# Kernel tuning notes

Hardware: AMD Instinct MI355X
Metric: run time of the kernel (lower is better)

The kernel has to match this reference:

```python
import math
import jax, jax.numpy as jnp
import numpy as np

B, N, D = 32, 1025, 768
K, CD, TD = 64, 128, 256  # num_clusters, cluster_dim, token_dim
REG = 0.1
NUM_ITERS = 5


def setup_inputs() -> dict:
    key = jax.random.key(0)
    ks = jax.random.split(key, 8)
    x = jax.random.normal(ks[0], (B, N, D), dtype=jnp.float32)
    # Linear params (torch nn.Linear: y = x @ W.T + b; we store W already transposed as [in, out])
    Wf = jax.random.normal(ks[1], (D, CD), dtype=jnp.float32) / math.sqrt(D)
    bf = jnp.zeros((CD,), dtype=jnp.float32)
    Ws = jax.random.normal(ks[2], (D, K), dtype=jnp.float32) / math.sqrt(D)
    bs = jnp.zeros((K,), dtype=jnp.float32)
    Wt = jax.random.normal(ks[3], (D, TD), dtype=jnp.float32) / math.sqrt(D)
    bt = jnp.zeros((TD,), dtype=jnp.float32)
    anchors = jax.random.normal(ks[4], (K, CD), dtype=jnp.float32) * 0.1
    dust_bin = jnp.float32(1.0)
    sharpness = jnp.float32(5.0)
    return {"x": x, "Wf": Wf, "bf": bf, "Ws": Ws, "bs": bs, "Wt": Wt, "bt": bt,
            "anchors": anchors, "dust_bin": dust_bin, "sharpness": sharpness}


def _log_otp_solver(log_a, log_b, M, num_iters, reg):
    M = M / reg
    u = jnp.zeros_like(log_a)  # [B, K+1]
    v = jnp.zeros_like(log_b)  # [B, N-1]
    for _ in range(num_iters):
        u = log_a - jax.nn.logsumexp(M + v[:, None, :], axis=2)
        v = log_b - jax.nn.logsumexp(M + u[:, :, None], axis=1)
    return M + u[:, :, None] + v[:, None, :]


def reference(x, Wf, bf, Ws, bs, Wt, bt, anchors, dust_bin, sharpness):
    b, n, d = x.shape
    t_global = x[:, 0]            # [B, D]
    fi = x[:, 1:]                 # [B, N-1, D]
    f = fi @ Wf + bf              # [B, N-1, CD]
    s = jnp.swapaxes(fi @ Ws + bs, 1, 2)  # [B, K, N-1]
    t = t_global @ Wt + bt        # [B, TD]
    s = s * sharpness
    dust = jnp.broadcast_to(dust_bin, (b, 1, n - 1))
    s_aug = jnp.concatenate([s, dust], axis=1)  # [B, K+1, N-1]
    log_a = jnp.full((b, K + 1), -math.log(K + 1), dtype=x.dtype)
    log_b = jnp.full((b, n - 1), -math.log(n - 1), dtype=x.dtype)
    log_P = _log_otp_solver(log_a, log_b, s_aug, NUM_ITERS, REG)
    p = jnp.exp(log_P)[:, :-1, :]  # [B, K, N-1]
    # v_agg = sum_n p[b,k,n] * (2*f[b,n,:] - anchors[k,:])  (algebraic rewrite of the broadcast sum)
    v_agg = 2.0 * jnp.einsum('bkn,bnc->bkc', p, f) - p.sum(axis=2)[:, :, None] * anchors[None]
    v_local = v_agg.reshape(b, -1)            # [B, K*CD]
    f_out = jnp.concatenate([t, v_local], axis=-1)
    norm = jnp.maximum(jnp.linalg.norm(f_out, axis=-1, keepdims=True), 1e-12)
    return f_out / norm
```

## Files before the change

### kernel.cpp

```cpp
#include <hip/hip_runtime.h>
#include <math.h>


#define BATCH 32
#define NTOK  1025
#define DIM   768
#define KDIM  64
#define CDIM  128
#define TDIM  256
#define NM1   1024
#define ROWLEN 8448
#define NITER 5
#define INV_REG 10.0f
#define NSPLIT 32
#define LOG_A (-4.17438727f)
#define LOG_B (-6.93147181f)

typedef __attribute__((ext_vector_type(8))) short short8;
typedef __attribute__((ext_vector_type(4))) float floatx4;

typedef __attribute__((address_space(3))) unsigned int lds_uint;
typedef const __attribute__((address_space(1))) unsigned int glb_uint;

__device__ __forceinline__ void gload_lds16(const void* g, void* l) {
    __builtin_amdgcn_global_load_lds((glb_uint*)g, (lds_uint*)l, 16, 0, 0);
}

__device__ __forceinline__ unsigned short bf16_rne(float f) {
    unsigned u = __builtin_bit_cast(unsigned, f);
    unsigned r = u + 0x7FFFu + ((u >> 16) & 1u);
    return (unsigned short)(r >> 16);
}

__device__ __forceinline__ short8 cvt8(float4 a, float4 b) {
    short8 r;
    r[0] = (short)bf16_rne(a.x); r[1] = (short)bf16_rne(a.y);
    r[2] = (short)bf16_rne(a.z); r[3] = (short)bf16_rne(a.w);
    r[4] = (short)bf16_rne(b.x); r[5] = (short)bf16_rne(b.y);
    r[6] = (short)bf16_rne(b.z); r[7] = (short)bf16_rne(b.w);
    return r;
}

__global__ __launch_bounds__(256) void pack_w(
    const float* __restrict__ Wf, const float* __restrict__ Ws,
    const float* __restrict__ bf, const float* __restrict__ bs,
    short* __restrict__ W_pack, float* __restrict__ bias_all)
{
    int idx = blockIdx.x * 256 + threadIdx.x;
    if (idx < 24 * 12 * 512) {
        int g    = idx / 6144;
        int rem  = idx - g * 6144;
        int nf   = rem >> 9;
        int rem2 = rem & 511;
        int lane = rem2 >> 3;
        int j    = rem2 & 7;
        int k = g * 32 + (lane >> 4) * 8 + j;
        int c = nf * 16 + (lane & 15);
        float v = (c < CDIM) ? Wf[(size_t)k * CDIM + c] : Ws[(size_t)k * KDIM + (c - CDIM)];
        W_pack[idx] = (short)bf16_rne(v);
    }
    if (idx < 192) bias_all[idx] = (idx < CDIM) ? bf[idx] : bs[idx - CDIM];
}

__global__ __launch_bounds__(256, 2) void gemm_fs(
    const float* __restrict__ x, const short* __restrict__ W_pack,
    const float* __restrict__ bias_all, const float* __restrict__ sharp_p,
    float* __restrict__ fmat, float* __restrict__ Mmat)
{
    __shared__ __align__(16) short Bs[12288];
    __shared__ __align__(16) short As[4096];
    const int tid  = threadIdx.x;
    const int wave = tid >> 6, lane = tid & 63;
    const int quad = lane >> 4, lrow = lane & 15;
    const int R = blockIdx.x * 64 + wave * 16;

    const int arow = blockIdx.x * 64 + (tid >> 2);
    const float* asrc = x + ((size_t)(arow >> 10) * NTOK + 1 + (arow & 1023)) * DIM + (tid & 3) * 16;
    const int r    = (tid >> 2) & 15;
    const int seg  = tid & 3;
    const int kk_w = seg >> 1;
    const int q0   = (seg & 1) * 2;
    short* adst0 = &As[(((tid >> 6) * 2 + kk_w) * 64 + q0 * 16 + r) * 8];
    short* adst1 = &As[(((tid >> 6) * 2 + kk_w) * 64 + (q0 + 1) * 16 + r) * 8];

    floatx4 acc[12];
#pragma unroll
    for (int nf = 0; nf < 12; ++nf) acc[nf] = (floatx4){0.f, 0.f, 0.f, 0.f};

    float4 g0 = *(const float4*)(asrc);
    float4 g1 = *(const float4*)(asrc + 4);
    float4 g2 = *(const float4*)(asrc + 8);
    float4 g3 = *(const float4*)(asrc + 12);

    for (int ko = 0; ko < 12; ++ko) {
        __syncthreads();
        const short* bsrc = W_pack + ko * 12288 + tid * 8;
#pragma unroll
        for (int i = 0; i < 6; ++i)
            gload_lds16(bsrc + i * 2048, &Bs[i * 2048 + tid * 8]);
        *(short8*)adst0 = cvt8(g0, g1);
        *(short8*)adst1 = cvt8(g2, g3);
        if (ko < 11) {
            const float* ap = asrc + (ko + 1) * 64;
            g0 = *(const float4*)(ap);
            g1 = *(const float4*)(ap + 4);
            g2 = *(const float4*)(ap + 8);
            g3 = *(const float4*)(ap + 12);
        }
        __syncthreads();
#pragma unroll
        for (int kk = 0; kk < 2; ++kk) {
            short8 af = *(const short8*)&As[((wave * 2 + kk) * 64 + lane) * 8];
#pragma unroll
            for (int nf = 0; nf < 12; ++nf) {
                short8 bf8 = *(const short8*)&Bs[((kk * 12 + nf) * 64 + lane) * 8];
                acc[nf] = __builtin_amdgcn_mfma_f32_16x16x32_bf16(af, bf8, acc[nf], 0, 0, 0);
            }
        }
    }

    const float sc = sharp_p[0] * INV_REG;
    const int bb = R >> 10;
    const int n0 = (R & 1023) + quad * 4;
#pragma unroll
    for (int nf = 0; nf < 12; ++nf) {
        const int c = nf * 16 + lrow;
        const float bias = bias_all[c];
        if (nf < 8) {
            float* fp = fmat + ((size_t)R + quad * 4) * CDIM + c;
#pragma unroll
            for (int j = 0; j < 4; ++j)
                fp[(size_t)j * CDIM] = acc[nf][j] + bias;
        } else {
            const int k = c - CDIM;
            float4 w = make_float4((acc[nf][0] + bias) * sc, (acc[nf][1] + bias) * sc,
                                   (acc[nf][2] + bias) * sc, (acc[nf][3] + bias) * sc);
            *(float4*)(Mmat + ((size_t)bb * KDIM + k) * NM1 + n0) = w;
        }
    }
}

__global__ __launch_bounds__(256) void gemm_t_split(
    const float* __restrict__ x, const float* __restrict__ Wt,
    float* __restrict__ tpart)
{
    __shared__ float xr[256];
    const int b = blockIdx.x, dy = blockIdx.y, c = threadIdx.x;
    xr[c] = x[(size_t)b * NTOK * DIM + (size_t)dy * 256 + c];
    __syncthreads();
    float acc = 0.f;
    const float* wp = Wt + (size_t)dy * 256 * TDIM + c;
#pragma unroll 8
    for (int d = 0; d < 256; ++d) acc = fmaf(xr[d], wp[(size_t)d * TDIM], acc);
    tpart[((size_t)dy * BATCH + b) * TDIM + c] = acc;
}

template<bool FIRST>
__global__ __launch_bounds__(256) void sink_u(
    const float* __restrict__ Mmat, const float* __restrict__ v_in,
    const float* __restrict__ dust_p, float* __restrict__ u_out)
{
    const int wv   = (blockIdx.x << 2) + (threadIdx.x >> 6);
    const int lane = threadIdx.x & 63;
    const int b = wv / 65, k = wv - b * 65;
    const float dustM = dust_p[0] * INV_REG;

    const float4* vp = (const float4*)(v_in + (size_t)b * NM1);
    float xs[16];
    if (k < 64) {
        const float4* Mp = (const float4*)(Mmat + ((size_t)b * KDIM + k) * NM1);
#pragma unroll
        for (int i = 0; i < 4; ++i) {
            float4 mv = Mp[i * 64 + lane];
            float4 vv = FIRST ? make_float4(0.f, 0.f, 0.f, 0.f) : vp[i * 64 + lane];
            xs[i * 4 + 0] = mv.x + vv.x;
            xs[i * 4 + 1] = mv.y + vv.y;
            xs[i * 4 + 2] = mv.z + vv.z;
            xs[i * 4 + 3] = mv.w + vv.w;
        }
    } else {
#pragma unroll
        for (int i = 0; i < 4; ++i) {
            float4 vv = FIRST ? make_float4(0.f, 0.f, 0.f, 0.f) : vp[i * 64 + lane];
            xs[i * 4 + 0] = dustM + vv.x;
            xs[i * 4 + 1] = dustM + vv.y;
            xs[i * 4 + 2] = dustM + vv.z;
            xs[i * 4 + 3] = dustM + vv.w;
        }
    }
    float m = xs[0];
#pragma unroll
    for (int i = 1; i < 16; ++i) m = fmaxf(m, xs[i]);
#pragma unroll
    for (int off = 1; off < 64; off <<= 1) m = fmaxf(m, __shfl_xor(m, off));
    float S = 0.f;
#pragma unroll
    for (int i = 0; i < 16; ++i) S += __expf(xs[i] - m);
#pragma unroll
    for (int off = 1; off < 64; off <<= 1) S += __shfl_xor(S, off);
    if (lane == 0) u_out[wv] = LOG_A - (m + __logf(S));
}

__global__ __launch_bounds__(128) void sink_v(
    const float* __restrict__ Mmat, const float* __restrict__ u_in,
    const float* __restrict__ dust_p, float* __restrict__ v_out)
{
    __shared__ float us[65];
    const int b = blockIdx.x, tid = threadIdx.x;
    const int n = blockIdx.y * 128 + tid;
    if (tid < 65) us[tid] = u_in[b * 65 + tid];
    __syncthreads();
    const float* Mb = Mmat + (size_t)b * KDIM * NM1 + n;
    float xs[64];
#pragma unroll
    for (int k = 0; k < 64; ++k) xs[k] = Mb[(size_t)k * NM1] + us[k];
    const float xd = dust_p[0] * INV_REG + us[64];
    float m = xd;
#pragma unroll
    for (int k = 0; k < 64; ++k) m = fmaxf(m, xs[k]);
    float S = __expf(xd - m);
#pragma unroll
    for (int k = 0; k < 64; ++k) S += __expf(xs[k] - m);
    v_out[(size_t)b * NM1 + n] = LOG_B - (m + __logf(S));
}

__global__ __launch_bounds__(256) void aggregate(
    const float* __restrict__ Mmat, const float* __restrict__ fmat,
    const float* __restrict__ u_in, const float* __restrict__ v_in,
    float* __restrict__ vpart, float* __restrict__ rspart)
{
    __shared__ float fs[32 * 128];
    __shared__ float ps[32 * 68];
    __shared__ float us[KDIM];
    __shared__ float vsh[32];
    const int b = blockIdx.x, ns = blockIdx.y;
    const int tid = threadIdx.x;
    const int tx = tid & 7;
    const int ty = tid >> 3;
    const int n0 = ns * 32;

    if (tid < 64) us[tid] = u_in[b * 65 + tid];
    else if (tid < 96) vsh[tid - 64] = v_in[(size_t)b * NM1 + n0 + (tid - 64)];
    __syncthreads();

    const float* fb = fmat + ((size_t)b * NM1 + n0) * CDIM;
#pragma unroll
    for (int q = 0; q < 4; ++q) {
        int idx = q * 256 + tid;
        int nn = idx >> 5, c4 = (idx & 31) * 4;
        *(float4*)&fs[nn * 128 + c4] = *(const float4*)(fb + (size_t)nn * CDIM + c4);
    }
    {
        const int p_nn = tid & 31, p_kb = tid >> 5;
        const float* Mb = Mmat + (size_t)b * KDIM * NM1 + n0 + p_nn;
        const float vv = vsh[p_nn];
#pragma unroll
        for (int q = 0; q < 8; ++q) {
            int k = q * 8 + p_kb;
            ps[p_nn * 68 + k] = __expf(Mb[(size_t)k * NM1] + us[k] + vv);
        }
    }
    __syncthreads();

    float rsacc = 0.f;
    if (tid < 64) {
#pragma unroll
        for (int nn = 0; nn < 32; ++nn) rsacc += ps[nn * 68 + tid];
    }
    float acc[8][4];
#pragma unroll
    for (int i = 0; i < 8; ++i)
#pragma unroll
        for (int j = 0; j < 4; ++j) acc[i][j] = 0.f;
#pragma unroll
    for (int nn = 0; nn < 32; ++nn) {
        float4 p0 = *(const float4*)&ps[nn * 68 + tx * 8];
        float4 p1 = *(const float4*)&ps[nn * 68 + tx * 8 + 4];
        float4 f0 = *(const float4*)&fs[nn * 128 + ty * 4];
        float pv[8] = {p0.x, p0.y, p0.z, p0.w, p1.x, p1.y, p1.z, p1.w};
        float fv[4] = {f0.x, f0.y, f0.z, f0.w};
#pragma unroll
        for (int i = 0; i < 8; ++i)
#pragma unroll
            for (int j = 0; j < 4; ++j)
                acc[i][j] = fmaf(pv[i], fv[j], acc[i][j]);
    }

    float* vp = vpart + (size_t)(ns * BATCH + b) * (KDIM * CDIM);
#pragma unroll
    for (int i = 0; i < 8; ++i) {
        int k = tx * 8 + i;
        *(float4*)(vp + (size_t)k * CDIM + ty * 4) =
            make_float4(acc[i][0], acc[i][1], acc[i][2], acc[i][3]);
    }
    if (tid < 64) rspart[(ns * BATCH + b) * KDIM + tid] = rsacc;
}

__global__ __launch_bounds__(256) void reduce_vagg(
    const float* __restrict__ vpart, const float* __restrict__ rspart,
    const float* __restrict__ anchors, float* __restrict__ vagg,
    float* __restrict__ sq)
{
    __shared__ float rst[8];
    __shared__ float red[4];
    const int b = blockIdx.x, segi = blockIdx.y, tid = threadIdx.x;
    const int lane = tid & 63, wave = tid >> 6;
    if (tid < 8) {
        float s = 0.f;
#pragma unroll
        for (int ns = 0; ns < NSPLIT; ++ns)
            s += rspart[(ns * BATCH + b) * KDIM + segi * 8 + tid];
        rst[tid] = s;
    }
    __syncthreads();
    const int i4 = segi * 256 + tid;
    float4 s = make_float4(0.f, 0.f, 0.f, 0.f);
#pragma unroll
    for (int ns = 0; ns < NSPLIT; ++ns) {
        const float4 v = *(const float4*)&vpart[(size_t)(ns * BATCH + b) * (KDIM * CDIM) + (size_t)i4 * 4];
        s.x += v.x; s.y += v.y; s.z += v.z; s.w += v.w;
    }
    float rs = rst[tid >> 5];
    const float4 an = *(const float4*)&anchors[(size_t)i4 * 4];
    float4 v;
    v.x = 2.f * s.x - rs * an.x;
    v.y = 2.f * s.y - rs * an.y;
    v.z = 2.f * s.z - rs * an.z;
    v.w = 2.f * s.w - rs * an.w;
    *(float4*)&vagg[(size_t)b * (KDIM * CDIM) + (size_t)i4 * 4] = v;
    float ss = v.x * v.x + v.y * v.y + v.z * v.z + v.w * v.w;
#pragma unroll
    for (int off = 32; off > 0; off >>= 1) ss += __shfl_down(ss, off);
    if (lane == 0) red[wave] = ss;
    __syncthreads();
    if (tid == 0) sq[b * 8 + segi] = red[0] + red[1] + red[2] + red[3];
}

__global__ __launch_bounds__(256) void finalize2(
    const float* __restrict__ tpart, const float* __restrict__ bt,
    const float* __restrict__ sq, const float* __restrict__ vagg,
    float* __restrict__ out)
{
    __shared__ float red[4];
    __shared__ float sc_sh;
    const int b = blockIdx.x, tid = threadIdx.x;
    const int lane = tid & 63, wave = tid >> 6;

    float t = bt[tid];
#pragma unroll
    for (int s = 0; s < 3; ++s) t += tpart[((size_t)s * BATCH + b) * TDIM + tid];
    float ss = t * t;
#pragma unroll
    for (int off = 32; off > 0; off >>= 1) ss += __shfl_down(ss, off);
    if (lane == 0) red[wave] = ss;
    __syncthreads();
    if (tid == 0) {
        float tot = red[0] + red[1] + red[2] + red[3];
#pragma unroll
        for (int i = 0; i < 8; ++i) tot += sq[b * 8 + i];
        sc_sh = 1.f / fmaxf(sqrtf(tot), 1e-12f);
    }
    __syncthreads();
    const float scale = sc_sh;
    float* orow = out + (size_t)b * ROWLEN;
    orow[tid] = t * scale;
    const float* va = vagg + (size_t)b * (KDIM * CDIM);
#pragma unroll
    for (int q = 0; q < 8; ++q) {
        int i4 = q * 256 + tid;
        float4 v = *(const float4*)&va[(size_t)i4 * 4];
        v.x *= scale; v.y *= scale; v.z *= scale; v.w *= scale;
        *(float4*)&orow[TDIM + (size_t)i4 * 4] = v;
    }
}

extern "C" void kernel_launch(void* const* d_in, const int* in_sizes, int n_in,
                              void* d_out, int out_size, void* d_ws, size_t ws_size,
                              hipStream_t stream)
{
    const float* x       = (const float*)d_in[0];
    const float* Wf      = (const float*)d_in[1];
    const float* bf      = (const float*)d_in[2];
    const float* Ws      = (const float*)d_in[3];
    const float* bs      = (const float*)d_in[4];
    const float* Wt      = (const float*)d_in[5];
    const float* bt      = (const float*)d_in[6];
    const float* anchors = (const float*)d_in[7];
    const float* dust    = (const float*)d_in[8];
    const float* sharp   = (const float*)d_in[9];
    float* out = (float*)d_out;

    char* base = (char*)d_ws;
    short* W_pack   = (short*)base;
    float* bias_all = (float*)(base + 294912);
    float* Mmat     = bias_all + 192;
    float* fmat     = Mmat + (size_t)BATCH * KDIM * NM1;
    float* u_buf    = fmat + (size_t)BATCH * NM1 * CDIM;
    float* v_buf    = u_buf + BATCH * 65;
    float* vpart    = v_buf + BATCH * NM1;
    float* rspart   = vpart + (size_t)NSPLIT * BATCH * KDIM * CDIM;
    float* tpart    = rspart + NSPLIT * BATCH * KDIM;
    float* sq       = tpart + 3 * BATCH * TDIM;
    float* vagg     = Mmat;

    hipLaunchKernelGGL(pack_w, dim3(576), dim3(256), 0, stream,
                       Wf, Ws, bf, bs, W_pack, bias_all);
    hipLaunchKernelGGL(gemm_fs, dim3(512), dim3(256), 0, stream,
                       x, W_pack, bias_all, sharp, fmat, Mmat);
    hipLaunchKernelGGL(gemm_t_split, dim3(BATCH, 3), dim3(256), 0, stream,
                       x, Wt, tpart);

    hipLaunchKernelGGL(HIP_KERNEL_NAME(sink_u<true>), dim3(520), dim3(256), 0, stream,
                       Mmat, v_buf, dust, u_buf);
    hipLaunchKernelGGL(sink_v, dim3(BATCH, 8), dim3(128), 0, stream,
                       Mmat, u_buf, dust, v_buf);
    for (int it = 1; it < NITER; ++it) {
        hipLaunchKernelGGL(HIP_KERNEL_NAME(sink_u<false>), dim3(520), dim3(256), 0, stream,
                           Mmat, v_buf, dust, u_buf);
        hipLaunchKernelGGL(sink_v, dim3(BATCH, 8), dim3(128), 0, stream,
                           Mmat, u_buf, dust, v_buf);
    }

    hipLaunchKernelGGL(aggregate, dim3(BATCH, NSPLIT), dim3(256), 0, stream,
                       Mmat, fmat, u_buf, v_buf, vpart, rspart);
    hipLaunchKernelGGL(reduce_vagg, dim3(BATCH, 8), dim3(256), 0, stream,
                       vpart, rspart, anchors, vagg, sq);
    hipLaunchKernelGGL(finalize2, dim3(BATCH), dim3(256), 0, stream,
                       tpart, bt, sq, vagg, out);
}
```

Before: 248.1 us.

## Use bf16 MFMA in aggregate with transposed bf16 features and fused finalize

The f projection is stored as transposed bf16 (fT), so the aggregation p·f runs on bf16 MFMA instructions instead of fp32 FMA, with P computed in registers. The N-split drops from 32 to 8, which reduces partial-sum traffic. The vagg reduction, anchor correction, norm and output write are fused into a single 1024-thread finalize kernel, and the t GEMM is merged into the weight-pack kernel, cutting launches. Rounding P and f to bf16 reduces accuracy, and the fewer aggregate blocks (256) lower parallelism.

```diff
diff --git a/kernel.cpp b/kernel.cpp
--- a/kernel.cpp
+++ b/kernel.cpp
@@ -12,7 +12,7 @@
 #define ROWLEN 8448
 #define NITER 5
 #define INV_REG 10.0f
-#define NSPLIT 32
+#define NS_AGG 8
 #define LOG_A (-4.17438727f)
 #define LOG_B (-6.93147181f)
 
@@ -41,13 +41,17 @@
     return r;
 }
 
-__global__ __launch_bounds__(256) void pack_w(
+__global__ __launch_bounds__(256) void prep(
     const float* __restrict__ Wf, const float* __restrict__ Ws,
     const float* __restrict__ bf, const float* __restrict__ bs,
-    short* __restrict__ W_pack, float* __restrict__ bias_all)
-{
-    int idx = blockIdx.x * 256 + threadIdx.x;
-    if (idx < 24 * 12 * 512) {
+    const float* __restrict__ x, const float* __restrict__ Wt,
+    short* __restrict__ W_pack, float* __restrict__ bias_all,
+    float* __restrict__ tpart)
+{
+    __shared__ float xr[256];
+    const int blk = blockIdx.x, tid = threadIdx.x;
+    if (blk < 576) {
+        int idx = blk * 256 + tid;
         int g    = idx / 6144;
         int rem  = idx - g * 6144;
         int nf   = rem >> 9;
@@ -58,14 +62,24 @@
         int c = nf * 16 + (lane & 15);
         float v = (c < CDIM) ? Wf[(size_t)k * CDIM + c] : Ws[(size_t)k * KDIM + (c - CDIM)];
         W_pack[idx] = (short)bf16_rne(v);
-    }
-    if (idx < 192) bias_all[idx] = (idx < CDIM) ? bf[idx] : bs[idx - CDIM];
+        if (idx < 192) bias_all[idx] = (idx < CDIM) ? bf[idx] : bs[idx - CDIM];
+    } else {
+        int i = blk - 576;
+        int b = i / 3, dy = i - b * 3;
+        xr[tid] = x[(size_t)b * NTOK * DIM + (size_t)dy * 256 + tid];
+        __syncthreads();
+        float acc = 0.f;
+        const float* wp = Wt + (size_t)dy * 256 * TDIM + tid;
+#pragma unroll 8
+        for (int d = 0; d < 256; ++d) acc = fmaf(xr[d], wp[(size_t)d * TDIM], acc);
+        tpart[((size_t)dy * BATCH + b) * TDIM + tid] = acc;
+    }
 }
 
 __global__ __launch_bounds__(256, 2) void gemm_fs(
     const float* __restrict__ x, const short* __restrict__ W_pack,
     const float* __restrict__ bias_all, const float* __restrict__ sharp_p,
-    float* __restrict__ fmat, float* __restrict__ Mmat)
+    unsigned short* __restrict__ fT, float* __restrict__ Mmat)
 {
     __shared__ __align__(16) short Bs[12288];
     __shared__ __align__(16) short As[4096];
@@ -121,38 +135,25 @@
 
     const float sc = sharp_p[0] * INV_REG;
     const int bb = R >> 10;
-    const int n0 = (R & 1023) + quad * 4;
+    const int tok = (R & 1023) + quad * 4;
 #pragma unroll
     for (int nf = 0; nf < 12; ++nf) {
         const int c = nf * 16 + lrow;
         const float bias = bias_all[c];
         if (nf < 8) {
-            float* fp = fmat + ((size_t)R + quad * 4) * CDIM + c;
-#pragma unroll
-            for (int j = 0; j < 4; ++j)
-                fp[(size_t)j * CDIM] = acc[nf][j] + bias;
+            ushort4 w;
+            w.x = bf16_rne(acc[nf][0] + bias);
+            w.y = bf16_rne(acc[nf][1] + bias);
+            w.z = bf16_rne(acc[nf][2] + bias);
+            w.w = bf16_rne(acc[nf][3] + bias);
+            *(ushort4*)(fT + ((size_t)bb * CDIM + c) * NM1 + tok) = w;
         } else {
             const int k = c - CDIM;
             float4 w = make_float4((acc[nf][0] + bias) * sc, (acc[nf][1] + bias) * sc,
                                    (acc[nf][2] + bias) * sc, (acc[nf][3] + bias) * sc);
-            *(float4*)(Mmat + ((size_t)bb * KDIM + k) * NM1 + n0) = w;
-        }
-    }
-}
-
-__global__ __launch_bounds__(256) void gemm_t_split(
-    const float* __restrict__ x, const float* __restrict__ Wt,
-    float* __restrict__ tpart)
-{
-    __shared__ float xr[256];
-    const int b = blockIdx.x, dy = blockIdx.y, c = threadIdx.x;
-    xr[c] = x[(size_t)b * NTOK * DIM + (size_t)dy * 256 + c];
-    __syncthreads();
-    float acc = 0.f;
-    const float* wp = Wt + (size_t)dy * 256 * TDIM + c;
-#pragma unroll 8
-    for (int d = 0; d < 256; ++d) acc = fmaf(xr[d], wp[(size_t)d * TDIM], acc);
-    tpart[((size_t)dy * BATCH + b) * TDIM + c] = acc;
+            *(float4*)(Mmat + ((size_t)bb * KDIM + k) * NM1 + tok) = w;
+        }
+    }
 }
 
 template<bool FIRST>
@@ -225,153 +226,142 @@
 }
 
 __global__ __launch_bounds__(256) void aggregate(
-    const float* __restrict__ Mmat, const float* __restrict__ fmat,
+    const float* __restrict__ Mmat, const unsigned short* __restrict__ fT,
     const float* __restrict__ u_in, const float* __restrict__ v_in,
     float* __restrict__ vpart, float* __restrict__ rspart)
 {
-    __shared__ float fs[32 * 128];
-    __shared__ float ps[32 * 68];
     __shared__ float us[KDIM];
-    __shared__ float vsh[32];
+    __shared__ float vsh[128];
     const int b = blockIdx.x, ns = blockIdx.y;
     const int tid = threadIdx.x;
-    const int tx = tid & 7;
-    const int ty = tid >> 3;
-    const int n0 = ns * 32;
+    const int wave = tid >> 6, lane = tid & 63;
+    const int quad = lane >> 4, lrow = lane & 15;
 
     if (tid < 64) us[tid] = u_in[b * 65 + tid];
-    else if (tid < 96) vsh[tid - 64] = v_in[(size_t)b * NM1 + n0 + (tid - 64)];
+    else if (tid < 192) vsh[tid - 64] = v_in[(size_t)b * NM1 + ns * 128 + (tid - 64)];
     __syncthreads();
 
-    const float* fb = fmat + ((size_t)b * NM1 + n0) * CDIM;
-#pragma unroll
-    for (int q = 0; q < 4; ++q) {
-        int idx = q * 256 + tid;
-        int nn = idx >> 5, c4 = (idx & 31) * 4;
-        *(float4*)&fs[nn * 128 + c4] = *(const float4*)(fb + (size_t)nn * CDIM + c4);
-    }
-    {
-        const int p_nn = tid & 31, p_kb = tid >> 5;
-        const float* Mb = Mmat + (size_t)b * KDIM * NM1 + n0 + p_nn;
-        const float vv = vsh[p_nn];
-#pragma unroll
-        for (int q = 0; q < 8; ++q) {
-            int k = q * 8 + p_kb;
-            ps[p_nn * 68 + k] = __expf(Mb[(size_t)k * NM1] + us[k] + vv);
-        }
-    }
-    __syncthreads();
-
-    float rsacc = 0.f;
-    if (tid < 64) {
-#pragma unroll
-        for (int nn = 0; nn < 32; ++nn) rsacc += ps[nn * 68 + tid];
-    }
-    float acc[8][4];
-#pragma unroll
-    for (int i = 0; i < 8; ++i)
-#pragma unroll
-        for (int j = 0; j < 4; ++j) acc[i][j] = 0.f;
-#pragma unroll
-    for (int nn = 0; nn < 32; ++nn) {
-        float4 p0 = *(const float4*)&ps[nn * 68 + tx * 8];
-        float4 p1 = *(const float4*)&ps[nn * 68 + tx * 8 + 4];
-        float4 f0 = *(const float4*)&fs[nn * 128 + ty * 4];
-        float pv[8] = {p0.x, p0.y, p0.z, p0.w, p1.x, p1.y, p1.z, p1.w};
-        float fv[4] = {f0.x, f0.y, f0.z, f0.w};
-#pragma unroll
-        for (int i = 0; i < 8; ++i)
-#pragma unroll
-            for (int j = 0; j < 4; ++j)
-                acc[i][j] = fmaf(pv[i], fv[j], acc[i][j]);
-    }
+    const int krow = wave * 16 + lrow;
+    const float uk = us[krow];
+    const float* Mrow = Mmat + ((size_t)b * KDIM + krow) * NM1 + ns * 128 + quad * 8;
+    const unsigned short* fbase = fT + ((size_t)b * CDIM + lrow) * NM1 + ns * 128 + quad * 8;
+
+    floatx4 acc[8];
+#pragma unroll
+    for (int nf = 0; nf < 8; ++nf) acc[nf] = (floatx4){0.f, 0.f, 0.f, 0.f};
+    float rs = 0.f;
+
+#pragma unroll
+    for (int step = 0; step < 4; ++step) {
+        const float* mp = Mrow + step * 32;
+        float4 m0 = *(const float4*)(mp);
+        float4 m1 = *(const float4*)(mp + 4);
+        const int tb = step * 32 + quad * 8;
+        float p[8];
+        p[0] = __expf(m0.x + uk + vsh[tb + 0]);
+        p[1] = __expf(m0.y + uk + vsh[tb + 1]);
+        p[2] = __expf(m0.z + uk + vsh[tb + 2]);
+        p[3] = __expf(m0.w + uk + vsh[tb + 3]);
+        p[4] = __expf(m1.x + uk + vsh[tb + 4]);
+        p[5] = __expf(m1.y + uk + vsh[tb + 5]);
+        p[6] = __expf(m1.z + uk + vsh[tb + 6]);
+        p[7] = __expf(m1.w + uk + vsh[tb + 7]);
+        short8 afrag;
+#pragma unroll
+        for (int j = 0; j < 8; ++j) {
+            rs += p[j];
+            afrag[j] = (short)bf16_rne(p[j]);
+        }
+#pragma unroll
+        for (int nf = 0; nf < 8; ++nf) {
+            short8 bfrag = *(const short8*)(fbase + (size_t)nf * 16 * NM1 + step * 32);
+            acc[nf] = __builtin_amdgcn_mfma_f32_16x16x32_bf16(afrag, bfrag, acc[nf], 0, 0, 0);
+        }
+    }
+
+    rs += __shfl_xor(rs, 16);
+    rs += __shfl_xor(rs, 32);
+    if (lane < 16) rspart[(ns * BATCH + b) * KDIM + krow] = rs;
 
     float* vp = vpart + (size_t)(ns * BATCH + b) * (KDIM * CDIM);
 #pragma unroll
-    for (int i = 0; i < 8; ++i) {
-        int k = tx * 8 + i;
-        *(float4*)(vp + (size_t)k * CDIM + ty * 4) =
-            make_float4(acc[i][0], acc[i][1], acc[i][2], acc[i][3]);
-    }
-    if (tid < 64) rspart[(ns * BATCH + b) * KDIM + tid] = rsacc;
-}
-
-__global__ __launch_bounds__(256) void reduce_vagg(
+    for (int nf = 0; nf < 8; ++nf) {
+        const int c = nf * 16 + lrow;
+#pragma unroll
+        for (int j = 0; j < 4; ++j)
+            vp[(size_t)(wave * 16 + quad * 4 + j) * CDIM + c] = acc[nf][j];
+    }
+}
+
+__global__ __launch_bounds__(1024) void finalize_all(
     const float* __restrict__ vpart, const float* __restrict__ rspart,
-    const float* __restrict__ anchors, float* __restrict__ vagg,
-    float* __restrict__ sq)
-{
-    __shared__ float rst[8];
-    __shared__ float red[4];
-    const int b = blockIdx.x, segi = blockIdx.y, tid = threadIdx.x;
-    const int lane = tid & 63, wave = tid >> 6;
-    if (tid < 8) {
-        float s = 0.f;
-#pragma unroll
-        for (int ns = 0; ns < NSPLIT; ++ns)
-            s += rspart[(ns * BATCH + b) * KDIM + segi * 8 + tid];
-        rst[tid] = s;
-    }
-    __syncthreads();
-    const int i4 = segi * 256 + tid;
-    float4 s = make_float4(0.f, 0.f, 0.f, 0.f);
-#pragma unroll
-    for (int ns = 0; ns < NSPLIT; ++ns) {
-        const float4 v = *(const float4*)&vpart[(size_t)(ns * BATCH + b) * (KDIM * CDIM) + (size_t)i4 * 4];
-        s.x += v.x; s.y += v.y; s.z += v.z; s.w += v.w;
-    }
-    float rs = rst[tid >> 5];
-    const float4 an = *(const float4*)&anchors[(size_t)i4 * 4];
-    float4 v;
-    v.x = 2.f * s.x - rs * an.x;
-    v.y = 2.f * s.y - rs * an.y;
-    v.z = 2.f * s.z - rs * an.z;
-    v.w = 2.f * s.w - rs * an.w;
-    *(float4*)&vagg[(size_t)b * (KDIM * CDIM) + (size_t)i4 * 4] = v;
-    float ss = v.x * v.x + v.y * v.y + v.z * v.z + v.w * v.w;
-#pragma unroll
-    for (int off = 32; off > 0; off >>= 1) ss += __shfl_down(ss, off);
-    if (lane == 0) red[wave] = ss;
-    __syncthreads();
-    if (tid == 0) sq[b * 8 + segi] = red[0] + red[1] + red[2] + red[3];
-}
-
-__global__ __launch_bounds__(256) void finalize2(
-    const float* __restrict__ tpart, const float* __restrict__ bt,
-    const float* __restrict__ sq, const float* __restrict__ vagg,
-    float* __restrict__ out)
-{
-    __shared__ float red[4];
+    const float* __restrict__ anchors, const float* __restrict__ tpart,
+    const float* __restrict__ bt, float* __restrict__ out)
+{
+    __shared__ float rstot[KDIM];
+    __shared__ float red[16];
     __shared__ float sc_sh;
     const int b = blockIdx.x, tid = threadIdx.x;
     const int lane = tid & 63, wave = tid >> 6;
 
-    float t = bt[tid];
-#pragma unroll
-    for (int s = 0; s < 3; ++s) t += tpart[((size_t)s * BATCH + b) * TDIM + tid];
-    float ss = t * t;
+    if (tid < KDIM) {
+        float s = 0.f;
+#pragma unroll
+        for (int ns = 0; ns < NS_AGG; ++ns)
+            s += rspart[(ns * BATCH + b) * KDIM + tid];
+        rstot[tid] = s;
+    }
+    __syncthreads();
+
+    const size_t e0 = (size_t)tid * 8;
+    float4 s0 = make_float4(0.f, 0.f, 0.f, 0.f);
+    float4 s1 = make_float4(0.f, 0.f, 0.f, 0.f);
+#pragma unroll
+    for (int ns = 0; ns < NS_AGG; ++ns) {
+        const float* vp = vpart + (size_t)(ns * BATCH + b) * (KDIM * CDIM) + e0;
+        float4 a = *(const float4*)(vp);
+        float4 c = *(const float4*)(vp + 4);
+        s0.x += a.x; s0.y += a.y; s0.z += a.z; s0.w += a.w;
+        s1.x += c.x; s1.y += c.y; s1.z += c.z; s1.w += c.w;
+    }
+    const float rsv = rstot[tid >> 4];
+    float4 a0 = *(const float4*)(anchors + e0);
+    float4 a1 = *(const float4*)(anchors + e0 + 4);
+    float4 v0, v1;
+    v0.x = 2.f * s0.x - rsv * a0.x;  v0.y = 2.f * s0.y - rsv * a0.y;
+    v0.z = 2.f * s0.z - rsv * a0.z;  v0.w = 2.f * s0.w - rsv * a0.w;
+    v1.x = 2.f * s1.x - rsv * a1.x;  v1.y = 2.f * s1.y - rsv * a1.y;
+    v1.z = 2.f * s1.z - rsv * a1.z;  v1.w = 2.f * s1.w - rsv * a1.w;
+    float ss = v0.x*v0.x + v0.y*v0.y + v0.z*v0.z + v0.w*v0.w
+             + v1.x*v1.x + v1.y*v1.y + v1.z*v1.z + v1.w*v1.w;
+
+    float t = 0.f;
+    if (tid < TDIM) {
+        t = bt[tid];
+#pragma unroll
+        for (int s = 0; s < 3; ++s) t += tpart[((size_t)s * BATCH + b) * TDIM + tid];
+        ss += t * t;
+    }
+
 #pragma unroll
     for (int off = 32; off > 0; off >>= 1) ss += __shfl_down(ss, off);
     if (lane == 0) red[wave] = ss;
     __syncthreads();
     if (tid == 0) {
-        float tot = red[0] + red[1] + red[2] + red[3];
-#pragma unroll
-        for (int i = 0; i < 8; ++i) tot += sq[b * 8 + i];
+        float tot = 0.f;
+#pragma unroll
+        for (int i = 0; i < 16; ++i) tot += red[i];
         sc_sh = 1.f / fmaxf(sqrtf(tot), 1e-12f);
     }
     __syncthreads();
     const float scale = sc_sh;
+
     float* orow = out + (size_t)b * ROWLEN;
-    orow[tid] = t * scale;
-    const float* va = vagg + (size_t)b * (KDIM * CDIM);
-#pragma unroll
-    for (int q = 0; q < 8; ++q) {
-        int i4 = q * 256 + tid;
-        float4 v = *(const float4*)&va[(size_t)i4 * 4];
-        v.x *= scale; v.y *= scale; v.z *= scale; v.w *= scale;
-        *(float4*)&orow[TDIM + (size_t)i4 * 4] = v;
-    }
+    if (tid < TDIM) orow[tid] = t * scale;
+    v0.x *= scale; v0.y *= scale; v0.z *= scale; v0.w *= scale;
+    v1.x *= scale; v1.y *= scale; v1.z *= scale; v1.w *= scale;
+    *(float4*)&orow[TDIM + e0]     = v0;
+    *(float4*)&orow[TDIM + e0 + 4] = v1;
 }
 
 extern "C" void kernel_launch(void* const* d_in, const int* in_sizes, int n_in,
@@ -391,24 +381,20 @@
     float* out = (float*)d_out;
 
     char* base = (char*)d_ws;
-    short* W_pack   = (short*)base;
-    float* bias_all = (float*)(base + 294912);
-    float* Mmat     = bias_all + 192;
-    float* fmat     = Mmat + (size_t)BATCH * KDIM * NM1;
-    float* u_buf    = fmat + (size_t)BATCH * NM1 * CDIM;
-    float* v_buf    = u_buf + BATCH * 65;
-    float* vpart    = v_buf + BATCH * NM1;
-    float* rspart   = vpart + (size_t)NSPLIT * BATCH * KDIM * CDIM;
-    float* tpart    = rspart + NSPLIT * BATCH * KDIM;
-    float* sq       = tpart + 3 * BATCH * TDIM;
-    float* vagg     = Mmat;
-
-    hipLaunchKernelGGL(pack_w, dim3(576), dim3(256), 0, stream,
-                       Wf, Ws, bf, bs, W_pack, bias_all);
+    short* W_pack        = (short*)base;
+    float* bias_all      = (float*)(base + 294912);
+    float* Mmat          = bias_all + 192;
+    unsigned short* fT   = (unsigned short*)(Mmat + (size_t)BATCH * KDIM * NM1);
+    float* u_buf         = (float*)(fT + (size_t)BATCH * CDIM * NM1);
+    float* v_buf         = u_buf + BATCH * 65;
+    float* vpart         = v_buf + BATCH * NM1;
+    float* rspart        = vpart + (size_t)NS_AGG * BATCH * KDIM * CDIM;
+    float* tpart         = rspart + NS_AGG * BATCH * KDIM;
+
+    hipLaunchKernelGGL(prep, dim3(672), dim3(256), 0, stream,
+                       Wf, Ws, bf, bs, x, Wt, W_pack, bias_all, tpart);
     hipLaunchKernelGGL(gemm_fs, dim3(512), dim3(256), 0, stream,
-                       x, W_pack, bias_all, sharp, fmat, Mmat);
-    hipLaunchKernelGGL(gemm_t_split, dim3(BATCH, 3), dim3(256), 0, stream,
-                       x, Wt, tpart);
+                       x, W_pack, bias_all, sharp, fT, Mmat);
 
     hipLaunchKernelGGL(HIP_KERNEL_NAME(sink_u<true>), dim3(520), dim3(256), 0, stream,
                        Mmat, v_buf, dust, u_buf);
@@ -421,10 +407,8 @@
                            Mmat, u_buf, dust, v_buf);
     }
 
-    hipLaunchKernelGGL(aggregate, dim3(BATCH, NSPLIT), dim3(256), 0, stream,
-                       Mmat, fmat, u_buf, v_buf, vpart, rspart);
-    hipLaunchKernelGGL(reduce_vagg, dim3(BATCH, 8), dim3(256), 0, stream,
-                       vpart, rspart, anchors, vagg, sq);
-    hipLaunchKernelGGL(finalize2, dim3(BATCH), dim3(256), 0, stream,
-                       tpart, bt, sq, vagg, out);
-}
+    hipLaunchKernelGGL(aggregate, dim3(BATCH, NS_AGG), dim3(256), 0, stream,
+                       Mmat, fT, u_buf, v_buf, vpart, rspart);
+    hipLaunchKernelGGL(finalize_all, dim3(BATCH), dim3(1024), 0, stream,
+                       vpart, rspart, anchors, tpart, bt, out);
+}
```

After: 242.2 us. 1.02x faster.
